# Kernel tuning notes

Measured on AMD Instinct MI355X. Metric: run time of the kernel, lower is better.

## Reference

```python
import jax, jax.numpy as jnp
import numpy as np

L = 2        # gnn_layers
D = 256      # hidden_dim
E = 1024     # emb_dim
NCLS = 7
NEG = 1e30


def lstm_cell(x, h, c, Wih, Whh, bih, bhh):
    # torch.nn.LSTMCell math; gate order i, f, g, o
    g = x @ Wih.T + bih + h @ Whh.T + bhh
    i, f, gg, o = jnp.split(g, 4, axis=-1)
    c2 = jax.nn.sigmoid(f) * c + jax.nn.sigmoid(i) * jnp.tanh(gg)
    return jax.nn.sigmoid(o) * jnp.tanh(c2), c2


def dag_layer(Hl, adj_f, W1, W2, Wr, Wc_ih, Wc_hh, bc_ih, bc_hh, Wp_ih, Wp_hh, bp_ih, bp_hh):
    # Hl: (B,N,D). Sequential DAG recurrence with dot-product attention over growing prefix.
    B, N, Dh = Hl.shape
    zeros = jnp.zeros((B, Dh), Hl.dtype)
    h0 = Hl[:, 0]
    C0, _ = lstm_cell(h0, zeros, zeros, Wc_ih, Wc_hh, bc_ih, bc_hh)
    P0, _ = lstm_cell(zeros, h0, h0, Wp_ih, Wp_hh, bp_ih, bp_hh)
    Ht0 = C0 + P0
    # carry pre-projected keys/values incrementally to avoid O(N^2 D^2) work
    K2 = jnp.zeros((B, N, Dh), Hl.dtype).at[:, 0].set(Ht0 @ W2.T)
    Vr = jnp.zeros((B, N, Dh), Hl.dtype).at[:, 0].set(Ht0 @ Wr.T)
    H1 = jnp.zeros((B, N, Dh), Hl.dtype).at[:, 0].set(Ht0)
    pos = jnp.arange(N)

    def step(carry, i):
        K2, Vr, H1 = carry
        Q = jax.lax.dynamic_index_in_dim(Hl, i, axis=1, keepdims=False)      # (B,D)
        adj_i = jax.lax.dynamic_index_in_dim(adj_f, i, axis=1, keepdims=False)  # (B,N)
        q = Q @ W1.T
        logits = jnp.einsum('bd,bnd->bn', q, K2) - (1.0 - adj_i) * NEG  # mask_logic
        logits = jnp.where(pos[None, :] < i, logits, -NEG)              # only prefix :i
        w = jax.nn.softmax(logits, axis=-1)
        M = jnp.einsum('bn,bnd->bd', w, Vr)
        C, _ = lstm_cell(Q, M, M, Wc_ih, Wc_hh, bc_ih, bc_hh)
        P, _ = lstm_cell(M, Q, Q, Wp_ih, Wp_hh, bp_ih, bp_hh)
        Ht = C + P
        K2 = K2.at[:, i].set(Ht @ W2.T)
        Vr = Vr.at[:, i].set(Ht @ Wr.T)
        H1 = H1.at[:, i].set(Ht)
        return (K2, Vr, H1), None

    (K2, Vr, H1), _ = jax.lax.scan(step, (K2, Vr, H1), jnp.arange(1, N))
    return H1


def setup_inputs() -> dict:
    key = jax.random.key(0)
    ks = iter(jax.random.split(key, 40))
    B, N = 16, 128
    s = lambda *sh: jax.random.normal(next(ks), sh, jnp.float32) * 0.02
    in_dim = D * (L + 1) + E
    return dict(
        features=jax.random.normal(next(ks), (B, N, E), jnp.float32),
        adj=jnp.ones((B, N, N), jnp.int32),
        s_mask=jnp.zeros((B, N, N), jnp.int32),
        s_mask_onehot=jnp.zeros((B, N, N, 2), jnp.int32),
        lengths=jnp.ones((B,), jnp.int32) * N,
        fc1_W=s(D, E), fc1_b=jnp.zeros((D,), jnp.float32),
        W1=s(L, D, D), W2=s(L, D, D), Wr=s(L, D, D),
        Wc_ih=s(L, 4 * D, D), Wc_hh=s(L, 4 * D, D),
        bc_ih=jnp.zeros((L, 4 * D), jnp.float32), bc_hh=jnp.zeros((L, 4 * D), jnp.float32),
        Wp_ih=s(L, 4 * D, D), Wp_hh=s(L, 4 * D, D),
        bp_ih=jnp.zeros((L, 4 * D), jnp.float32), bp_hh=jnp.zeros((L, 4 * D), jnp.float32),
        m0_W=s(D, in_dim), m0_b=jnp.zeros((D,), jnp.float32),
        m1_W=s(D, D), m1_b=jnp.zeros((D,), jnp.float32),
        m2_W=s(NCLS, D), m2_b=jnp.zeros((NCLS,), jnp.float32),
    )


def reference(features, adj, s_mask, s_mask_onehot, lengths,
              fc1_W, fc1_b, W1, W2, Wr,
              Wc_ih, Wc_hh, bc_ih, bc_hh,
              Wp_ih, Wp_hh, bp_ih, bp_hh,
              m0_W, m0_b, m1_W, m1_b, m2_W, m2_b):
    # s_mask / s_mask_onehot unused for attn_type='dotprod', no_rel_attn=True
    # lengths unused for nodal_att_type=None (attentive_node_features is identity)
    adj_f = adj.astype(features.dtype)
    H0 = jax.nn.relu(features @ fc1_W.T + fc1_b)
    Hs = [H0]
    for l in range(L):
        Hs.append(dag_layer(Hs[l], adj_f,
                            W1[l], W2[l], Wr[l],
                            Wc_ih[l], Wc_hh[l], bc_ih[l], bc_hh[l],
                            Wp_ih[l], Wp_hh[l], bp_ih[l], bp_hh[l]))
    Hcat = jnp.concatenate(Hs + [features], axis=2)  # (B,N,D*(L+1)+E)
    h = jax.nn.relu(Hcat @ m0_W.T + m0_b)
    h = jax.nn.relu(h @ m1_W.T + m1_b)  # mlp_layers-1 extra layer; dropout p=0 -> identity
    return h @ m2_W.T + m2_b            # (B,N,num_class)
```

## Files before the change

### kernel.cpp

```cpp
#include <hip/hip_runtime.h>
#include <math.h>

#define B_ 16
#define N_ 128
#define D_ 256
#define E_ 1024
#define GD4 1024

template<bool BIAS, bool RELU>
__global__ __launch_bounds__(256) void gemm_k(const float* __restrict__ X,
    const float* __restrict__ W, const float* __restrict__ bias,
    float* __restrict__ C, int M, int N, int K)
{
  __shared__ float Xs[32][68];
  __shared__ float Ws[32][68];
  const int tid = threadIdx.x;
  const int m0 = blockIdx.x * 64, n0 = blockIdx.y * 64;
  const int tm = tid >> 4, tn = tid & 15;
  float acc[4][4] = {};
  for (int k0 = 0; k0 < K; k0 += 32) {
    for (int e = tid; e < 2048; e += 256) {
      int mm = e >> 5, kk = e & 31;
      Xs[kk][mm] = X[(m0+mm)*K + k0+kk];
    }
    for (int e = tid; e < 2048; e += 256) {
      int nn = e >> 5, kk = e & 31;
      Ws[kk][nn] = (n0+nn < N) ? W[(n0+nn)*K + k0+kk] : 0.f;
    }
    __syncthreads();
    for (int kk = 0; kk < 32; kk++) {
      float4 a = *(const float4*)&Xs[kk][tm*4];
      float4 b = *(const float4*)&Ws[kk][tn*4];
      acc[0][0] += a.x*b.x; acc[0][1] += a.x*b.y; acc[0][2] += a.x*b.z; acc[0][3] += a.x*b.w;
      acc[1][0] += a.y*b.x; acc[1][1] += a.y*b.y; acc[1][2] += a.y*b.z; acc[1][3] += a.y*b.w;
      acc[2][0] += a.z*b.x; acc[2][1] += a.z*b.y; acc[2][2] += a.z*b.z; acc[2][3] += a.z*b.w;
      acc[3][0] += a.w*b.x; acc[3][1] += a.w*b.y; acc[3][2] += a.w*b.z; acc[3][3] += a.w*b.w;
    }
    __syncthreads();
  }
  for (int i2 = 0; i2 < 4; i2++) {
    int row = m0 + tm*4 + i2;
    for (int j2 = 0; j2 < 4; j2++) {
      int col = n0 + tn*4 + j2;
      if (col < N) {
        float v = acc[i2][j2];
        if (BIAS) v += bias[col];
        if (RELU) v = fmaxf(v, 0.f);
        C[row*N + col] = v;
      }
    }
  }
}

__global__ __launch_bounds__(256) void prepamat_k(const float* __restrict__ W2,
    const float* __restrict__ W1, float* __restrict__ AM)
{
  __shared__ float Xs[32][68];
  __shared__ float Ws[32][68];
  const int tid = threadIdx.x;
  const int m0 = blockIdx.x * 64, n0 = blockIdx.y * 64;
  const float* X = W2 + blockIdx.z * 65536;
  const float* W = W1 + blockIdx.z * 65536;
  float* C = AM + blockIdx.z * 65536;
  const int tm = tid >> 4, tn = tid & 15;
  float acc[4][4] = {};
  for (int k0 = 0; k0 < 256; k0 += 32) {
    for (int e = tid; e < 2048; e += 256) {
      int kk = e >> 6, mm = e & 63;
      Xs[kk][mm] = X[(k0+kk)*256 + m0+mm];
    }
    for (int e = tid; e < 2048; e += 256) {
      int kk = e >> 6, nn = e & 63;
      Ws[kk][nn] = W[(k0+kk)*256 + n0+nn];
    }
    __syncthreads();
    for (int kk = 0; kk < 32; kk++) {
      float4 a = *(const float4*)&Xs[kk][tm*4];
      float4 b = *(const float4*)&Ws[kk][tn*4];
      acc[0][0] += a.x*b.x; acc[0][1] += a.x*b.y; acc[0][2] += a.x*b.z; acc[0][3] += a.x*b.w;
      acc[1][0] += a.y*b.x; acc[1][1] += a.y*b.y; acc[1][2] += a.y*b.z; acc[1][3] += a.y*b.w;
      acc[2][0] += a.z*b.x; acc[2][1] += a.z*b.y; acc[2][2] += a.z*b.z; acc[2][3] += a.z*b.w;
      acc[3][0] += a.w*b.x; acc[3][1] += a.w*b.y; acc[3][2] += a.w*b.z; acc[3][3] += a.w*b.w;
    }
    __syncthreads();
  }
  for (int i2 = 0; i2 < 4; i2++)
    for (int j2 = 0; j2 < 4; j2++)
      C[(m0 + tm*4 + i2)*256 + n0 + tn*4 + j2] = acc[i2][j2];
}

__global__ __launch_bounds__(256) void prepnn_k(const float* __restrict__ Wch,
    const float* __restrict__ Wpi, const float* __restrict__ Wr,
    float* __restrict__ OUT)
{
  __shared__ float Xs[32][68];
  __shared__ float Ws[32][68];
  const int tid = threadIdx.x;
  const int m0 = blockIdx.x * 64, n0 = blockIdx.y * 64;
  const int l = blockIdx.z;
  const float* X = (m0 < 1024) ? (Wch + l*262144 + m0*256)
                               : (Wpi + l*262144 + (m0-1024)*256);
  const float* W = Wr + l*65536;
  float* C = OUT + l*524288;
  const int tm = tid >> 4, tn = tid & 15;
  float acc[4][4] = {};
  for (int k0 = 0; k0 < 256; k0 += 32) {
    for (int e = tid; e < 2048; e += 256) {
      int mm = e >> 5, kk = e & 31;
      Xs[kk][mm] = X[mm*256 + k0+kk];
    }
    for (int e = tid; e < 2048; e += 256) {
      int kk = e >> 6, nn = e & 63;
      Ws[kk][nn] = W[(k0+kk)*256 + n0+nn];
    }
    __syncthreads();
    for (int kk = 0; kk < 32; kk++) {
      float4 a = *(const float4*)&Xs[kk][tm*4];
      float4 b = *(const float4*)&Ws[kk][tn*4];
      acc[0][0] += a.x*b.x; acc[0][1] += a.x*b.y; acc[0][2] += a.x*b.z; acc[0][3] += a.x*b.w;
      acc[1][0] += a.y*b.x; acc[1][1] += a.y*b.y; acc[1][2] += a.y*b.z; acc[1][3] += a.y*b.w;
      acc[2][0] += a.z*b.x; acc[2][1] += a.z*b.y; acc[2][2] += a.z*b.z; acc[2][3] += a.z*b.w;
      acc[3][0] += a.w*b.x; acc[3][1] += a.w*b.y; acc[3][2] += a.w*b.z; acc[3][3] += a.w*b.w;
    }
    __syncthreads();
  }
  for (int i2 = 0; i2 < 4; i2++)
    for (int j2 = 0; j2 < 4; j2++)
      C[(m0 + tm*4 + i2)*256 + n0 + tn*4 + j2] = acc[i2][j2];
}

__global__ void bias_sum_k(const float* __restrict__ bci, const float* __restrict__ bch,
                           const float* __restrict__ bpi, const float* __restrict__ bph,
                           float* __restrict__ bcC, float* __restrict__ bpC)
{
  int i = blockIdx.x*256 + threadIdx.x;
  if (i < 2048) { bcC[i] = bci[i] + bch[i]; bpC[i] = bpi[i] + bph[i]; }
}

__global__ void pack_k(const float* __restrict__ wchpi, const float* __restrict__ wr,
                       float* __restrict__ out)
{
  int idx = blockIdx.x*256 + threadIdx.x;
  int l  = idx / 589824; int r2 = idx % 589824;
  int sl = r2 / 36864;   int rem = r2 % 36864;
  int r  = rem / 4096;   int rem2 = rem % 4096;
  int o  = rem2 >> 10;   int t = (rem2 >> 2) & 255; int j = rem2 & 3;
  int d  = sl*16 + (t >> 4);
  int c  = o*64 + (t & 15)*4 + j;
  float v;
  if (r < 8) v = wchpi[l*524288 + (r*256 + d)*256 + c];
  else       v = wr[l*65536 + d*256 + c];
  out[idx] = v;
}

__global__ __launch_bounds__(256) void prologue_k(const float* __restrict__ X,
    const float* __restrict__ Wc, const float* __restrict__ Wp,
    const float* __restrict__ Am, const float* __restrict__ bcc,
    const float* __restrict__ bpc, float* __restrict__ GQC,
    float* __restrict__ GQP, float* __restrict__ VM)
{
  __shared__ float Xs[32][68];
  __shared__ float Ws[32][68];
  const int tid = threadIdx.x;
  const int m0 = blockIdx.x * 64;
  const int nt = blockIdx.y;
  const float* W; const float* bias; float* C; int n0; int NC;
  if (nt < 16)      { W = Wc; bias = bcc;     C = GQC; n0 = nt*64;      NC = 1024; }
  else if (nt < 32) { W = Wp; bias = bpc;     C = GQP; n0 = (nt-16)*64; NC = 1024; }
  else              { W = Am; bias = nullptr; C = VM;  n0 = (nt-32)*64; NC = 256;  }
  const int tm = tid >> 4, tn = tid & 15;
  float acc[4][4] = {};
  for (int k0 = 0; k0 < 256; k0 += 32) {
    for (int e = tid; e < 2048; e += 256) {
      int mm = e >> 5, kk = e & 31;
      Xs[kk][mm] = X[(m0+mm)*256 + k0+kk];
    }
    for (int e = tid; e < 2048; e += 256) {
      int nn = e >> 5, kk = e & 31;
      Ws[kk][nn] = W[(n0+nn)*256 + k0+kk];
    }
    __syncthreads();
    for (int kk = 0; kk < 32; kk++) {
      float4 a = *(const float4*)&Xs[kk][tm*4];
      float4 b = *(const float4*)&Ws[kk][tn*4];
      acc[0][0] += a.x*b.x; acc[0][1] += a.x*b.y; acc[0][2] += a.x*b.z; acc[0][3] += a.x*b.w;
      acc[1][0] += a.y*b.x; acc[1][1] += a.y*b.y; acc[1][2] += a.y*b.z; acc[1][3] += a.y*b.w;
      acc[2][0] += a.z*b.x; acc[2][1] += a.z*b.y; acc[2][2] += a.z*b.z; acc[2][3] += a.z*b.w;
      acc[3][0] += a.w*b.x; acc[3][1] += a.w*b.y; acc[3][2] += a.w*b.z; acc[3][3] += a.w*b.w;
    }
    __syncthreads();
  }
  for (int i2 = 0; i2 < 4; i2++) {
    int row = m0 + tm*4 + i2;
    for (int j2 = 0; j2 < 4; j2++) {
      int col = n0 + tn*4 + j2;
      float v = acc[i2][j2];
      if (bias) v += bias[col];
      C[row*NC + col] = v;
    }
  }
}

__global__ __launch_bounds__(256) void m0fused_k(const float* __restrict__ H0,
    const float* __restrict__ H1, const float* __restrict__ H2,
    const float* __restrict__ feat, const float* __restrict__ W,
    const float* __restrict__ bias, float* __restrict__ C)
{
  __shared__ float Xs[32][68];
  __shared__ float Ws[32][68];
  const int tid = threadIdx.x;
  const int m0 = blockIdx.x * 64, n0 = blockIdx.y * 64;
  const int tm = tid >> 4, tn = tid & 15;
  float acc[4][4] = {};
  for (int k0 = 0; k0 < 1792; k0 += 32) {
    for (int e = tid; e < 2048; e += 256) {
      int mm = e >> 5, kk = e & 31;
      int k = k0 + kk, row = m0 + mm;
      float v;
      if (k < 768) {
        const float* src = (k < 256) ? H0 : ((k < 512) ? H1 : H2);
        v = src[row*256 + (k & 255)];
      } else v = feat[row*1024 + (k - 768)];
      Xs[kk][mm] = v;
    }
    for (int e = tid; e < 2048; e += 256) {
      int nn = e >> 5, kk = e & 31;
      Ws[kk][nn] = W[(n0+nn)*1792 + k0+kk];
    }
    __syncthreads();
    for (int kk = 0; kk < 32; kk++) {
      float4 a = *(const float4*)&Xs[kk][tm*4];
      float4 b = *(const float4*)&Ws[kk][tn*4];
      acc[0][0] += a.x*b.x; acc[0][1] += a.x*b.y; acc[0][2] += a.x*b.z; acc[0][3] += a.x*b.w;
      acc[1][0] += a.y*b.x; acc[1][1] += a.y*b.y; acc[1][2] += a.y*b.z; acc[1][3] += a.y*b.w;
      acc[2][0] += a.z*b.x; acc[2][1] += a.z*b.y; acc[2][2] += a.z*b.z; acc[2][3] += a.z*b.w;
      acc[3][0] += a.w*b.x; acc[3][1] += a.w*b.y; acc[3][2] += a.w*b.z; acc[3][3] += a.w*b.w;
    }
    __syncthreads();
  }
  for (int i2 = 0; i2 < 4; i2++) {
    int row = m0 + tm*4 + i2;
    for (int j2 = 0; j2 < 4; j2++) {
      int col = n0 + tn*4 + j2;
      C[row*256 + col] = fmaxf(acc[i2][j2] + bias[col], 0.f);
    }
  }
}

__device__ __forceinline__ float sigf(float x) { return 1.f / (1.f + __expf(-x)); }
__device__ __forceinline__ float tanhfast(float x) {
  float xc = fminf(fmaxf(x, -15.f), 15.f);
  float e = __expf(-2.f * xc);
  return (1.f - e) / (1.f + e);
}

__global__ __launch_bounds__(512) void scan_k(
    const float* __restrict__ Hl,
    const float* __restrict__ Vm,
    const float* __restrict__ gqC,
    const float* __restrict__ gqP,
    const float* __restrict__ WTp,
    const int*   __restrict__ adj,
    float* __restrict__ Hout,
    unsigned* __restrict__ cnt)
{
  __shared__ float4 wl4[9216];
  __shared__ float s_lds[256];
  __shared__ float v_s[256];
  __shared__ float ssum[2][257];
  __shared__ float psum[128];
  __shared__ float aw[128];
  __shared__ int   adj_s[128];
  __shared__ float gqc_l[64];
  __shared__ float gqp_l[64];
  __shared__ float gsum[9][16];
  __shared__ float ql[16];

  const int tid = threadIdx.x;
  const int b   = blockIdx.x >> 4;
  const int sl  = blockIdx.x & 15;
  unsigned* myslot = cnt + (b*16 + sl)*32;

  { const float4* src = (const float4*)WTp + sl*9216;
    for (int e = tid; e < 9216; e += 512) wl4[e] = src[e]; }

  const int rr = tid >> 2;
  const int rj = tid & 3;
  const int th = tid >> 8;
  const int t8 = tid & 255;

  for (int i = 0; i < N_; ++i) {
    __syncthreads();
    if (tid < 256)       v_s[tid] = Vm[(b*N_ + i)*D_ + tid];
    else if (tid < 320)  { int u = tid-256; gqc_l[u] = gqC[(b*N_+i)*GD4 + (u>>4)*D_ + sl*16 + (u&15)]; }
    else if (tid < 384)  { int u = tid-320; gqp_l[u] = gqP[(b*N_+i)*GD4 + (u>>4)*D_ + sl*16 + (u&15)]; }
    else                 { int u = tid-384; adj_s[u] = adj[(b*N_ + i)*N_ + u]; }
    if (tid < 16) ql[tid] = Hl[(b*N_+i)*D_ + sl*16 + tid];

    if (i > 0) {
      float4 areg[16];
      const float4* hp = (const float4*)(Hout + ((size_t)(b*N_ + rr))*D_) + rj;
      if (rr + 1 < i) {
        #pragma unroll
        for (int c4 = 0; c4 < 16; ++c4) areg[c4] = hp[c4*4];
      }
      if (tid < 16) {
        unsigned* slot = cnt + (b*16 + tid)*32;
        while (__hip_atomic_load(slot, __ATOMIC_RELAXED, __HIP_MEMORY_SCOPE_AGENT) < (unsigned)i)
          __builtin_amdgcn_s_sleep(1);
      }
      __syncthreads();
      asm volatile("" ::: "memory");
      if (rr + 1 == i) {
        #pragma unroll
        for (int c4 = 0; c4 < 16; ++c4) areg[c4] = hp[c4*4];
      }
      {
        float acc = 0.f;
        if (rr < i) {
          const float4* vv = (const float4*)v_s + rj;
          #pragma unroll
          for (int c4 = 0; c4 < 16; ++c4) {
            float4 a = areg[c4];
            float4 w = vv[c4*4];
            acc += a.x*w.x + a.y*w.y + a.z*w.z + a.w*w.w;
          }
        }
        acc += __shfl_xor(acc, 1, 64);
        acc += __shfl_xor(acc, 2, 64);
        if (rj == 0) psum[rr] = acc;
      }
      __syncthreads();

      if (tid < 128)
        aw[tid] = ((tid < i) && (adj_s[tid] != 0)) ? __expf(psum[tid]) : 0.f;
      __syncthreads();

      {
        const float* hb = Hout + (size_t)b*N_*D_ + t8;
        int k0 = th ? (i >> 1) : 0;
        int k1 = th ? i : (i >> 1);
        float s0=0.f, s1=0.f, s2=0.f, s3=0.f, z=0.f;
        int kk = k0;
        for (; kk + 4 <= k1; kk += 4) {
          float a0=aw[kk+0], a1=aw[kk+1], a2=aw[kk+2], a3=aw[kk+3];
          z  += (a0+a1)+(a2+a3);
          s0 += a0 * hb[(kk+0)*D_];
          s1 += a1 * hb[(kk+1)*D_];
          s2 += a2 * hb[(kk+2)*D_];
          s3 += a3 * hb[(kk+3)*D_];
        }
        for (; kk < k1; ++kk) { float a=aw[kk]; z+=a; s0 += a*hb[kk*D_]; }
        ssum[th][t8] = (s0+s1) + (s2+s3);
        if (t8 == 0) ssum[th][256] = z;
      }
      __syncthreads();
      if (tid < 256) {
        float inv = 1.f / (ssum[0][256] + ssum[1][256]);
        s_lds[tid] = (ssum[0][tid] + ssum[1][tid]) * inv;
      }
      __syncthreads();

      {
        const float4* s4 = (const float4*)s_lds;
        float4 sv0 = s4[ 0 + (t8 & 15)];
        float4 sv1 = s4[16 + (t8 & 15)];
        float4 sv2 = s4[32 + (t8 & 15)];
        float4 sv3 = s4[48 + (t8 & 15)];
        float g0=0.f, g1=0.f, g2=0.f, g3=0.f, g4=0.f;
        #define ROWDOT(r) ({                                                 \
          float4 w0 = wl4[((r)*4+0)*256 + t8];                               \
          float4 w1 = wl4[((r)*4+1)*256 + t8];                               \
          float4 w2 = wl4[((r)*4+2)*256 + t8];                               \
          float4 w3 = wl4[((r)*4+3)*256 + t8];                               \
          w0.x*sv0.x + w0.y*sv0.y + w0.z*sv0.z + w0.w*sv0.w                  \
        + w1.x*sv1.x + w1.y*sv1.y + w1.z*sv1.z + w1.w*sv1.w                  \
        + w2.x*sv2.x + w2.y*sv2.y + w2.z*sv2.z + w2.w*sv2.w                  \
        + w3.x*sv3.x + w3.y*sv3.y + w3.z*sv3.z + w3.w*sv3.w; })
        if (th == 0) { g0 = ROWDOT(0); g1 = ROWDOT(1); g2 = ROWDOT(2); g3 = ROWDOT(3); }
        else         { g0 = ROWDOT(4); g1 = ROWDOT(5); g2 = ROWDOT(6); g3 = ROWDOT(7); g4 = ROWDOT(8); }
        #undef ROWDOT
        #pragma unroll
        for (int m = 1; m <= 8; m <<= 1) {
          g0 += __shfl_xor(g0, m, 64);
          g1 += __shfl_xor(g1, m, 64);
          g2 += __shfl_xor(g2, m, 64);
          g3 += __shfl_xor(g3, m, 64);
          g4 += __shfl_xor(g4, m, 64);
        }
        if ((t8 & 15) == 0) {
          int d = t8 >> 4;
          if (th == 0) { gsum[0][d]=g0; gsum[1][d]=g1; gsum[2][d]=g2; gsum[3][d]=g3; }
          else         { gsum[4][d]=g0; gsum[5][d]=g1; gsum[6][d]=g2; gsum[7][d]=g3; gsum[8][d]=g4; }
        }
      }
      __syncthreads();
    } else {
      if (tid < 144) gsum[tid >> 4][tid & 15] = 0.f;
      __syncthreads();
    }

    if (tid < 16) {
      int dl = tid;
      float Mv = gsum[8][dl];
      float Qv = ql[dl];
      float giC = gsum[0][dl] + gqc_l[ 0 + dl];
      float gfC = gsum[1][dl] + gqc_l[16 + dl];
      float ggC = gsum[2][dl] + gqc_l[32 + dl];
      float goC = gsum[3][dl] + gqc_l[48 + dl];
      float giP = gsum[4][dl] + gqp_l[ 0 + dl];
      float gfP = gsum[5][dl] + gqp_l[16 + dl];
      float ggP = gsum[6][dl] + gqp_l[32 + dl];
      float goP = gsum[7][dl] + gqp_l[48 + dl];
      float c2C = sigf(gfC)*Mv + sigf(giC)*tanhfast(ggC);
      float Cv  = sigf(goC)*tanhfast(c2C);
      float c2P = sigf(gfP)*Qv + sigf(giP)*tanhfast(ggP);
      float Pv  = sigf(goP)*tanhfast(c2P);
      float htv = Cv + Pv;
      int d = sl*16 + dl;
      __hip_atomic_store(&Hout[(b*N_ + i)*D_ + d], htv,
                         __ATOMIC_RELAXED, __HIP_MEMORY_SCOPE_AGENT);
    }
    if (tid == 0) {
      asm volatile("s_waitcnt vmcnt(0)" ::: "memory");
      __hip_atomic_fetch_add(myslot, 1u, __ATOMIC_RELAXED, __HIP_MEMORY_SCOPE_AGENT);
    }
  }
}

extern "C" void kernel_launch(void* const* d_in, const int* in_sizes, int n_in,
                              void* d_out, int out_size, void* d_ws, size_t ws_size,
                              hipStream_t stream)
{
  const float* features = (const float*)d_in[0];
  const int*   adj      = (const int*)  d_in[1];
  const float* fc1_W    = (const float*)d_in[5];
  const float* fc1_b    = (const float*)d_in[6];
  const float* W1       = (const float*)d_in[7];
  const float* W2       = (const float*)d_in[8];
  const float* Wr       = (const float*)d_in[9];
  const float* Wc_ih    = (const float*)d_in[10];
  const float* Wc_hh    = (const float*)d_in[11];
  const float* bc_ih    = (const float*)d_in[12];
  const float* bc_hh    = (const float*)d_in[13];
  const float* Wp_ih    = (const float*)d_in[14];
  const float* Wp_hh    = (const float*)d_in[15];
  const float* bp_ih    = (const float*)d_in[16];
  const float* bp_hh    = (const float*)d_in[17];
  const float* m0_W     = (const float*)d_in[18];
  const float* m0_b     = (const float*)d_in[19];
  const float* m1_W     = (const float*)d_in[20];
  const float* m1_b     = (const float*)d_in[21];
  const float* m2_W     = (const float*)d_in[22];
  const float* m2_b     = (const float*)d_in[23];

  float* ws = (float*)d_ws;
  float* WTP    = ws + 0;
  float* AMAT   = ws + 1179648;
  float* BCC    = ws + 1310720;
  float* BPC    = ws + 1312768;
  float* WCHPI  = ws + 1314816;
  float* H0     = ws + 2363392;
  float* H1     = ws + 2887680;
  float* H2     = ws + 3411968;
  float* VMAT   = ws + 3936256;
  float* GQC    = ws + 4460544;
  float* GQP    = ws + 6557696;
  unsigned* CNT = (unsigned*)(ws + 8654848);
  float* HB1    = ws + 8671232;
  float* HB2    = ws + 9195520;

  hipMemsetAsync(CNT, 0, 65536, stream);
  bias_sum_k<<<8, 256, 0, stream>>>(bc_ih, bc_hh, bp_ih, bp_hh, BCC, BPC);
  prepamat_k<<<dim3(4,4,2), 256, 0, stream>>>(W2, W1, AMAT);
  prepnn_k<<<dim3(32,4,2), 256, 0, stream>>>(Wc_hh, Wp_ih, Wr, WCHPI);
  pack_k<<<4608, 256, 0, stream>>>(WCHPI, Wr, WTP);

  gemm_k<true,true><<<dim3(32,4), 256, 0, stream>>>(features, fc1_W, fc1_b, H0, 2048, 256, 1024);

  prologue_k<<<dim3(32,36), 256, 0, stream>>>(H0, Wc_ih, Wp_hh, AMAT,
                                              BCC, BPC, GQC, GQP, VMAT);
  scan_k<<<256, 512, 0, stream>>>(H0, VMAT, GQC, GQP, WTP, adj, H1, CNT);

  prologue_k<<<dim3(32,36), 256, 0, stream>>>(H1, Wc_ih + 262144, Wp_hh + 262144,
                                              AMAT + 65536, BCC + 1024, BPC + 1024,
                                              GQC, GQP, VMAT);
  scan_k<<<256, 512, 0, stream>>>(H1, VMAT, GQC, GQP, WTP + 589824, adj, H2, CNT + 8192);

  m0fused_k<<<dim3(32,4), 256, 0, stream>>>(H0, H1, H2, features, m0_W, m0_b, HB1);
  gemm_k<true,true ><<<dim3(32,4), 256, 0, stream>>>(HB1, m1_W, m1_b, HB2, 2048, 256, 256);
  gemm_k<true,false><<<dim3(32,1), 256, 0, stream>>>(HB2, m2_W, m2_b, (float*)d_out, 2048, 7, 256);
}
```

Before: 1.976 ms.

## Cache per-row gate projections, use fp16 weights, sentinel-based sync and prefetch

The scan kernel now projects each new hidden row through the packed weights once, storing the 144-wide gate contributions in shared memory G. Each step's gates then become a softmax-weighted sum of cached rows instead of a weighted sum over the H prefix followed by a full matvec. Weights are packed as fp16 and evaluated with fdot2 to halve the LDS footprint. Per-block counters are replaced by sentinel-value polling on the output rows, and the next step's inputs are prefetched into double buffers. This removes the per-step 144x256 matvec over the aggregated state, a counter atomic and several barriers, at the cost of fp16 weight precision and reliance on a NaN sentinel never being produced as a real output.

Result: no change. 1.992 ms (+0.8%).

```diff
diff --git a/kernel.cpp b/kernel.cpp
--- a/kernel.cpp
+++ b/kernel.cpp
@@ -1,4 +1,5 @@
 #include <hip/hip_runtime.h>
+#include <hip/hip_fp16.h>
 #include <math.h>
 
 #define B_ 16
@@ -6,6 +7,9 @@
 #define D_ 256
 #define E_ 1024
 #define GD4 1024
+#define SENT 0xFFC0DEADu
+
+typedef _Float16 h2 __attribute__((ext_vector_type(2)));
 
 template<bool BIAS, bool RELU>
 __global__ __launch_bounds__(256) void gemm_k(const float* __restrict__ X,
@@ -138,19 +142,29 @@
 }
 
 __global__ void pack_k(const float* __restrict__ wchpi, const float* __restrict__ wr,
-                       float* __restrict__ out)
+                       _Float16* __restrict__ out)
 {
   int idx = blockIdx.x*256 + threadIdx.x;
-  int l  = idx / 589824; int r2 = idx % 589824;
-  int sl = r2 / 36864;   int rem = r2 % 36864;
-  int r  = rem / 4096;   int rem2 = rem % 4096;
-  int o  = rem2 >> 10;   int t = (rem2 >> 2) & 255; int j = rem2 & 3;
-  int d  = sl*16 + (t >> 4);
-  int c  = o*64 + (t & 15)*4 + j;
+  int l  = idx / 589824; int rem = idx % 589824;
+  int sl = rem / 36864;  int rem2 = rem % 36864;
+  int cq = rem2 / 1152;  int rem3 = rem2 % 1152;
+  int r  = rem3 >> 3;    int e = rem3 & 7;
+  int c  = cq*8 + e;
+  int g  = r >> 4, dl = r & 15;
+  int d  = sl*16 + dl;
   float v;
-  if (r < 8) v = wchpi[l*524288 + (r*256 + d)*256 + c];
+  if (g < 8) v = wchpi[l*524288 + (g*256 + d)*256 + c];
   else       v = wr[l*65536 + d*256 + c];
-  out[idx] = v;
+  out[idx] = (_Float16)v;
+}
+
+__global__ void fill_k(unsigned* __restrict__ a, unsigned* __restrict__ b)
+{
+  int i = blockIdx.x*256 + threadIdx.x;
+  if (i < 524288) {
+    __hip_atomic_store(a + i, SENT, __ATOMIC_RELAXED, __HIP_MEMORY_SCOPE_AGENT);
+    __hip_atomic_store(b + i, SENT, __ATOMIC_RELAXED, __HIP_MEMORY_SCOPE_AGENT);
+  }
 }
 
 __global__ __launch_bounds__(256) void prologue_k(const float* __restrict__ X,
@@ -253,179 +267,194 @@
   float e = __expf(-2.f * xc);
   return (1.f - e) / (1.f + e);
 }
-
-__global__ __launch_bounds__(512) void scan_k(
+__device__ __forceinline__ float dot2w(unsigned w, h2 hv, float acc) {
+#if __has_builtin(__builtin_amdgcn_fdot2)
+  return __builtin_amdgcn_fdot2(__builtin_bit_cast(h2, w), hv, acc, false);
+#else
+  union { unsigned u; _Float16 e[2]; } c; c.u = w;
+  return acc + (float)c.e[0]*(float)hv.x + (float)c.e[1]*(float)hv.y;
+#endif
+}
+__device__ __forceinline__ float dot2h(h2 a, h2 b, float acc) {
+#if __has_builtin(__builtin_amdgcn_fdot2)
+  return __builtin_amdgcn_fdot2(a, b, acc, false);
+#else
+  return acc + (float)a.x*(float)b.x + (float)a.y*(float)b.y;
+#endif
+}
+
+__global__ __launch_bounds__(512, 2) void scan_k(
     const float* __restrict__ Hl,
     const float* __restrict__ Vm,
     const float* __restrict__ gqC,
     const float* __restrict__ gqP,
-    const float* __restrict__ WTp,
+    const _Float16* __restrict__ WTp,
     const int*   __restrict__ adj,
-    float* __restrict__ Hout,
-    unsigned* __restrict__ cnt)
-{
-  __shared__ float4 wl4[9216];
-  __shared__ float s_lds[256];
+    float* __restrict__ Hout)
+{
+  __shared__ uint4 wl4[4608];
+  __shared__ float G[128*144];
+  __shared__ __align__(16) _Float16 h2s[256];
   __shared__ float v_s[256];
-  __shared__ float ssum[2][257];
+  __shared__ __align__(16) _Float16 v2s[256];
   __shared__ float psum[128];
   __shared__ float aw[128];
-  __shared__ int   adj_s[128];
-  __shared__ float gqc_l[64];
-  __shared__ float gqp_l[64];
-  __shared__ float gsum[9][16];
-  __shared__ float ql[16];
+  __shared__ int   adj_s[2][128];
+  __shared__ float gqc_l[2][64], gqp_l[2][64];
+  __shared__ float ql[2][16];
+  __shared__ float Gg[144];
+  __shared__ float red[2];
 
   const int tid = threadIdx.x;
   const int b   = blockIdx.x >> 4;
   const int sl  = blockIdx.x & 15;
-  unsigned* myslot = cnt + (b*16 + sl)*32;
-
-  { const float4* src = (const float4*)WTp + sl*9216;
-    for (int e = tid; e < 9216; e += 512) wl4[e] = src[e]; }
-
-  const int rr = tid >> 2;
-  const int rj = tid & 3;
-  const int th = tid >> 8;
-  const int t8 = tid & 255;
+
+  { const uint4* src = (const uint4*)WTp + (size_t)sl*4608;
+    for (int e = tid; e < 4608; e += 512) wl4[e] = src[e]; }
+
+  const int rr_ = tid >> 2;
+  const int rj  = tid & 3;
+
+#define PREF(ip_, bf_) do {                                                    \
+    int ip = (ip_); int bf = (bf_);                                            \
+    for (int u = tid - 288; u < 528; u += 224) {                               \
+      if (u < 256) { float v = Vm[(b*N_ + ip)*D_ + u]; v_s[u] = v;             \
+                     h2s[0] = h2s[0]; v2s[u] = (_Float16)v; }                  \
+      else if (u < 384) adj_s[bf][u-256] = adj[(b*N_ + ip)*N_ + (u-256)];      \
+      else if (u < 448) gqc_l[bf][u-384] = gqC[(b*N_+ip)*GD4 + ((u-384)>>4)*D_ + sl*16 + ((u-384)&15)]; \
+      else if (u < 512) gqp_l[bf][u-448] = gqP[(b*N_+ip)*GD4 + ((u-448)>>4)*D_ + sl*16 + ((u-448)&15)]; \
+      else ql[bf][u-512] = Hl[(b*N_+ip)*D_ + sl*16 + (u-512)];                 \
+    }                                                                          \
+  } while (0)
+
+  if (tid >= 288) PREF(0, 0);
+  __syncthreads();
 
   for (int i = 0; i < N_; ++i) {
-    __syncthreads();
-    if (tid < 256)       v_s[tid] = Vm[(b*N_ + i)*D_ + tid];
-    else if (tid < 320)  { int u = tid-256; gqc_l[u] = gqC[(b*N_+i)*GD4 + (u>>4)*D_ + sl*16 + (u&15)]; }
-    else if (tid < 384)  { int u = tid-320; gqp_l[u] = gqP[(b*N_+i)*GD4 + (u>>4)*D_ + sl*16 + (u&15)]; }
-    else                 { int u = tid-384; adj_s[u] = adj[(b*N_ + i)*N_ + u]; }
-    if (tid < 16) ql[tid] = Hl[(b*N_+i)*D_ + sl*16 + tid];
-
+    const int cur = i & 1;
     if (i > 0) {
       float4 areg[16];
-      const float4* hp = (const float4*)(Hout + ((size_t)(b*N_ + rr))*D_) + rj;
-      if (rr + 1 < i) {
+      const float4* hp = (const float4*)(Hout + ((size_t)(b*N_ + rr_))*D_) + rj;
+      if (rr_ + 1 < i) {
         #pragma unroll
         for (int c4 = 0; c4 < 16; ++c4) areg[c4] = hp[c4*4];
       }
       if (tid < 16) {
-        unsigned* slot = cnt + (b*16 + tid)*32;
-        while (__hip_atomic_load(slot, __ATOMIC_RELAXED, __HIP_MEMORY_SCOPE_AGENT) < (unsigned)i)
+        const unsigned* w = (const unsigned*)Hout
+                          + ((size_t)(b*N_ + (i-1)))*D_ + tid*16 + 15;
+        while (__hip_atomic_load(w, __ATOMIC_RELAXED, __HIP_MEMORY_SCOPE_AGENT) == SENT)
           __builtin_amdgcn_s_sleep(1);
       }
       __syncthreads();
       asm volatile("" ::: "memory");
-      if (rr + 1 == i) {
-        #pragma unroll
-        for (int c4 = 0; c4 < 16; ++c4) areg[c4] = hp[c4*4];
+
+      if (tid < 256) {
+        float hv = Hout[((size_t)(b*N_ + (i-1)))*D_ + tid];
+        h2s[tid] = (_Float16)hv;
       }
       {
         float acc = 0.f;
-        if (rr < i) {
+        if (rr_ + 1 < i) {
           const float4* vv = (const float4*)v_s + rj;
           #pragma unroll
           for (int c4 = 0; c4 < 16; ++c4) {
-            float4 a = areg[c4];
-            float4 w = vv[c4*4];
+            float4 a = areg[c4], w = vv[c4*4];
             acc += a.x*w.x + a.y*w.y + a.z*w.z + a.w*w.w;
           }
+          acc += __shfl_xor(acc, 1, 64);
+          acc += __shfl_xor(acc, 2, 64);
+          if (rj == 0) psum[rr_] = acc;
+        }
+      }
+      __syncthreads();
+
+      if (tid < 288) {
+        int r = tid >> 1, hf = tid & 1;
+        float acc = 0.f;
+        #pragma unroll 4
+        for (int it = 0; it < 16; ++it) {
+          int cq = hf*16 + it;
+          uint4 w4 = wl4[cq*144 + r];
+          const h2* hh = (const h2*)h2s + cq*4;
+          acc = dot2w(w4.x, hh[0], acc);
+          acc = dot2w(w4.y, hh[1], acc);
+          acc = dot2w(w4.z, hh[2], acc);
+          acc = dot2w(w4.w, hh[3], acc);
         }
         acc += __shfl_xor(acc, 1, 64);
+        if (!hf) G[(i-1)*144 + r] = acc;
+      }
+      if (rr_ == i-1) {
+        const h2* hh = (const h2*)h2s + rj*32;
+        const h2* vv = (const h2*)v2s + rj*32;
+        float acc = 0.f;
+        #pragma unroll 8
+        for (int q = 0; q < 32; ++q) acc = dot2h(hh[q], vv[q], acc);
+        acc += __shfl_xor(acc, 1, 64);
         acc += __shfl_xor(acc, 2, 64);
-        if (rj == 0) psum[rr] = acc;
+        if (rj == 0) psum[i-1] = acc;
+      }
+      if (tid >= 384) {
+        int k = tid - 384;
+        float e = (k + 1 < i && adj_s[cur][k] != 0) ? __expf(psum[k]) : 0.f;
+        aw[k] = e;
+        float sv = e;
+        #pragma unroll
+        for (int off = 32; off >= 1; off >>= 1) sv += __shfl_xor(sv, off, 64);
+        if ((k & 63) == 0) red[k >> 6] = sv;
       }
       __syncthreads();
 
-      if (tid < 128)
-        aw[tid] = ((tid < i) && (adj_s[tid] != 0)) ? __expf(psum[tid]) : 0.f;
-      __syncthreads();
-
-      {
-        const float* hb = Hout + (size_t)b*N_*D_ + t8;
-        int k0 = th ? (i >> 1) : 0;
-        int k1 = th ? i : (i >> 1);
-        float s0=0.f, s1=0.f, s2=0.f, s3=0.f, z=0.f;
-        int kk = k0;
-        for (; kk + 4 <= k1; kk += 4) {
-          float a0=aw[kk+0], a1=aw[kk+1], a2=aw[kk+2], a3=aw[kk+3];
-          z  += (a0+a1)+(a2+a3);
-          s0 += a0 * hb[(kk+0)*D_];
-          s1 += a1 * hb[(kk+1)*D_];
-          s2 += a2 * hb[(kk+2)*D_];
-          s3 += a3 * hb[(kk+3)*D_];
-        }
-        for (; kk < k1; ++kk) { float a=aw[kk]; z+=a; s0 += a*hb[kk*D_]; }
-        ssum[th][t8] = (s0+s1) + (s2+s3);
-        if (t8 == 0) ssum[th][256] = z;
-      }
-      __syncthreads();
-      if (tid < 256) {
-        float inv = 1.f / (ssum[0][256] + ssum[1][256]);
-        s_lds[tid] = (ssum[0][tid] + ssum[1][tid]) * inv;
-      }
-      __syncthreads();
-
-      {
-        const float4* s4 = (const float4*)s_lds;
-        float4 sv0 = s4[ 0 + (t8 & 15)];
-        float4 sv1 = s4[16 + (t8 & 15)];
-        float4 sv2 = s4[32 + (t8 & 15)];
-        float4 sv3 = s4[48 + (t8 & 15)];
-        float g0=0.f, g1=0.f, g2=0.f, g3=0.f, g4=0.f;
-        #define ROWDOT(r) ({                                                 \
-          float4 w0 = wl4[((r)*4+0)*256 + t8];                               \
-          float4 w1 = wl4[((r)*4+1)*256 + t8];                               \
-          float4 w2 = wl4[((r)*4+2)*256 + t8];                               \
-          float4 w3 = wl4[((r)*4+3)*256 + t8];                               \
-          w0.x*sv0.x + w0.y*sv0.y + w0.z*sv0.z + w0.w*sv0.w                  \
-        + w1.x*sv1.x + w1.y*sv1.y + w1.z*sv1.z + w1.w*sv1.w                  \
-        + w2.x*sv2.x + w2.y*sv2.y + w2.z*sv2.z + w2.w*sv2.w                  \
-        + w3.x*sv3.x + w3.y*sv3.y + w3.z*sv3.z + w3.w*sv3.w; })
-        if (th == 0) { g0 = ROWDOT(0); g1 = ROWDOT(1); g2 = ROWDOT(2); g3 = ROWDOT(3); }
-        else         { g0 = ROWDOT(4); g1 = ROWDOT(5); g2 = ROWDOT(6); g3 = ROWDOT(7); g4 = ROWDOT(8); }
-        #undef ROWDOT
-        #pragma unroll
-        for (int m = 1; m <= 8; m <<= 1) {
-          g0 += __shfl_xor(g0, m, 64);
-          g1 += __shfl_xor(g1, m, 64);
-          g2 += __shfl_xor(g2, m, 64);
-          g3 += __shfl_xor(g3, m, 64);
-          g4 += __shfl_xor(g4, m, 64);
-        }
-        if ((t8 & 15) == 0) {
-          int d = t8 >> 4;
-          if (th == 0) { gsum[0][d]=g0; gsum[1][d]=g1; gsum[2][d]=g2; gsum[3][d]=g3; }
-          else         { gsum[4][d]=g0; gsum[5][d]=g1; gsum[6][d]=g2; gsum[7][d]=g3; gsum[8][d]=g4; }
-        }
+      if (tid < 288) {
+        int r = tid >> 1, kh = tid & 1;
+        float e1 = (adj_s[cur][i-1] != 0) ? __expf(psum[i-1]) : 0.f;
+        float g = kh ? e1 * G[(i-1)*144 + r] : 0.f;
+        int m = i - 1;
+        int k0 = kh ? (m >> 1) : 0, k1 = kh ? m : (m >> 1);
+        for (int k = k0; k < k1; ++k) g += aw[k] * G[k*144 + r];
+        g += __shfl_xor(g, 1, 64);
+        if (!kh) Gg[r] = g;
+      } else {
+        PREF((i < 127) ? i+1 : 127, (i+1) & 1);
       }
       __syncthreads();
     } else {
-      if (tid < 144) gsum[tid >> 4][tid & 15] = 0.f;
+      if (tid >= 288) PREF(1, 1);
       __syncthreads();
     }
 
-    if (tid < 16) {
-      int dl = tid;
-      float Mv = gsum[8][dl];
-      float Qv = ql[dl];
-      float giC = gsum[0][dl] + gqc_l[ 0 + dl];
-      float gfC = gsum[1][dl] + gqc_l[16 + dl];
-      float ggC = gsum[2][dl] + gqc_l[32 + dl];
-      float goC = gsum[3][dl] + gqc_l[48 + dl];
-      float giP = gsum[4][dl] + gqp_l[ 0 + dl];
-      float gfP = gsum[5][dl] + gqp_l[16 + dl];
-      float ggP = gsum[6][dl] + gqp_l[32 + dl];
-      float goP = gsum[7][dl] + gqp_l[48 + dl];
-      float c2C = sigf(gfC)*Mv + sigf(giC)*tanhfast(ggC);
-      float Cv  = sigf(goC)*tanhfast(c2C);
-      float c2P = sigf(gfP)*Qv + sigf(giP)*tanhfast(ggP);
-      float Pv  = sigf(goP)*tanhfast(c2P);
-      float htv = Cv + Pv;
-      int d = sl*16 + dl;
-      __hip_atomic_store(&Hout[(b*N_ + i)*D_ + d], htv,
-                         __ATOMIC_RELAXED, __HIP_MEMORY_SCOPE_AGENT);
-    }
-    if (tid == 0) {
-      asm volatile("s_waitcnt vmcnt(0)" ::: "memory");
-      __hip_atomic_fetch_add(myslot, 1u, __ATOMIC_RELAXED, __HIP_MEMORY_SCOPE_AGENT);
-    }
-  }
+    if (tid < 32) {
+      int dl = tid >> 1, cell = tid & 1;
+      float inv = 0.f;
+      if (i > 0) {
+        float e1m = (adj_s[cur][i-1] != 0) ? __expf(psum[i-1]) : 0.f;
+        inv = 1.f / (red[0] + red[1] + e1m);
+      }
+      float r0 = 0.f, r1 = 0.f, r2 = 0.f, r3 = 0.f, Mv = 0.f;
+      if (i > 0) {
+        r0 = Gg[(cell*4+0)*16 + dl] * inv;
+        r1 = Gg[(cell*4+1)*16 + dl] * inv;
+        r2 = Gg[(cell*4+2)*16 + dl] * inv;
+        r3 = Gg[(cell*4+3)*16 + dl] * inv;
+        Mv = Gg[128 + dl] * inv;
+      }
+      float Qv = ql[cur][dl];
+      const float* gq = cell ? &gqp_l[cur][0] : &gqc_l[cur][0];
+      float xi = cell ? Qv : Mv;
+      float gi_ = r0 + gq[ 0 + dl];
+      float gf_ = r1 + gq[16 + dl];
+      float gg_ = r2 + gq[32 + dl];
+      float go_ = r3 + gq[48 + dl];
+      float c2  = sigf(gf_)*xi + sigf(gi_)*tanhfast(gg_);
+      float ov  = sigf(go_)*tanhfast(c2);
+      float htv = ov + __shfl_xor(ov, 1, 64);
+      if (!cell) {
+        __hip_atomic_store(&Hout[((size_t)(b*N_ + i))*D_ + sl*16 + dl], htv,
+                           __ATOMIC_RELAXED, __HIP_MEMORY_SCOPE_AGENT);
+      }
+    }
+  }
+#undef PREF
 }
 
 extern "C" void kernel_launch(void* const* d_in, const int* in_sizes, int n_in,
@@ -455,22 +484,21 @@
   const float* m2_b     = (const float*)d_in[23];
 
   float* ws = (float*)d_ws;
-  float* WTP    = ws + 0;
-  float* AMAT   = ws + 1179648;
-  float* BCC    = ws + 1310720;
-  float* BPC    = ws + 1312768;
-  float* WCHPI  = ws + 1314816;
-  float* H0     = ws + 2363392;
-  float* H1     = ws + 2887680;
-  float* H2     = ws + 3411968;
-  float* VMAT   = ws + 3936256;
-  float* GQC    = ws + 4460544;
-  float* GQP    = ws + 6557696;
-  unsigned* CNT = (unsigned*)(ws + 8654848);
-  float* HB1    = ws + 8671232;
-  float* HB2    = ws + 9195520;
-
-  hipMemsetAsync(CNT, 0, 65536, stream);
+  _Float16* WTP = (_Float16*)ws;
+  float* AMAT   = ws + 589824;
+  float* BCC    = ws + 720896;
+  float* BPC    = ws + 722944;
+  float* WCHPI  = ws + 724992;
+  float* H0     = ws + 1773568;
+  float* H1     = ws + 2297856;
+  float* H2     = ws + 2822144;
+  float* VMAT   = ws + 3346432;
+  float* GQC    = ws + 3870720;
+  float* GQP    = ws + 5967872;
+  float* HB1    = ws + 8065024;
+  float* HB2    = ws + 8589312;
+
+  fill_k<<<2048, 256, 0, stream>>>((unsigned*)H1, (unsigned*)H2);
   bias_sum_k<<<8, 256, 0, stream>>>(bc_ih, bc_hh, bp_ih, bp_hh, BCC, BPC);
   prepamat_k<<<dim3(4,4,2), 256, 0, stream>>>(W2, W1, AMAT);
   prepnn_k<<<dim3(32,4,2), 256, 0, stream>>>(Wc_hh, Wp_ih, Wr, WCHPI);
@@ -480,12 +508,12 @@
 
   prologue_k<<<dim3(32,36), 256, 0, stream>>>(H0, Wc_ih, Wp_hh, AMAT,
                                               BCC, BPC, GQC, GQP, VMAT);
-  scan_k<<<256, 512, 0, stream>>>(H0, VMAT, GQC, GQP, WTP, adj, H1, CNT);
+  scan_k<<<256, 512, 0, stream>>>(H0, VMAT, GQC, GQP, WTP, adj, H1);
 
   prologue_k<<<dim3(32,36), 256, 0, stream>>>(H1, Wc_ih + 262144, Wp_hh + 262144,
                                               AMAT + 65536, BCC + 1024, BPC + 1024,
                                               GQC, GQP, VMAT);
-  scan_k<<<256, 512, 0, stream>>>(H1, VMAT, GQC, GQP, WTP + 589824, adj, H2, CNT + 8192);
+  scan_k<<<256, 512, 0, stream>>>(H1, VMAT, GQC, GQP, WTP + 589824, adj, H2);
 
   m0fused_k<<<dim3(32,4), 256, 0, stream>>>(H0, H1, H2, features, m0_W, m0_b, HB1);
   gemm_k<true,true ><<<dim3(32,4), 256, 0, stream>>>(HB1, m1_W, m1_b, HB2, 2048, 256, 256);
```
